# Kernel tuning notes

Hardware: AMD Instinct MI355X
Metric: run time of the kernel (lower is better)

## Reference

```python
import jax, jax.numpy as jnp
import numpy as np

NUM_HEAD = 16
DIM = 1024
T, B = 2048, 4


def setup_inputs() -> dict:
    key = jax.random.key(0)
    ks = jax.random.split(key, 12)
    s = 1.0 / np.sqrt(DIM)
    return {
        "x1": jax.random.normal(ks[0], (T, B, DIM), jnp.float32),
        "x2": jax.random.normal(ks[1], (T, B, DIM), jnp.float32),
        "Wq": jax.random.normal(ks[2], (DIM, DIM), jnp.float32) * s,
        "bq": jax.random.normal(ks[3], (DIM,), jnp.float32) * 0.01,
        "Wk": jax.random.normal(ks[4], (DIM, DIM), jnp.float32) * s,
        "bk": jax.random.normal(ks[5], (DIM,), jnp.float32) * 0.01,
        "Wv": jax.random.normal(ks[6], (DIM, DIM), jnp.float32) * s,
        "bv": jax.random.normal(ks[7], (DIM,), jnp.float32) * 0.01,
        "Wu": jax.random.normal(ks[8], (DIM, DIM), jnp.float32) * s,
        "bu": jax.random.normal(ks[9], (DIM,), jnp.float32) * 0.01,
    }


def reference(x1, x2, Wq, bq, Wk, bk, Wv, bv, Wu, bu):
    T1, B1, C = x1.shape
    T2 = x2.shape[0]
    H = NUM_HEAD
    hd = C // H
    # (T,B,C) -> (B,T,C)
    x1b = jnp.transpose(x1, (1, 0, 2))
    x2b = jnp.transpose(x2, (1, 0, 2))
    # torch Linear: y = x @ W.T + b
    q = (x1b @ Wq.T + bq).reshape(B1, T1, H, hd).transpose(0, 2, 1, 3)  # (B,H,T1,hd)
    k = (x2b @ Wk.T + bk).reshape(B1, T2, H, hd).transpose(0, 2, 1, 3)
    v = (x2b @ Wv.T + bv).reshape(B1, T2, H, hd).transpose(0, 2, 1, 3)
    # NOTE: source scales by 1/sqrt(C) (full dim), not 1/sqrt(head_dim)
    attn = jnp.einsum("bhqd,bhkd->bhqk", q, k) / jnp.sqrt(jnp.asarray(C, q.dtype))
    attn = jax.nn.softmax(attn, axis=-1)
    # dropout = identity (eval mode, deterministic reference)
    out = jnp.einsum("bhqk,bhkd->bhqd", attn, v)  # (B,H,T1,hd)
    out = out.transpose(0, 2, 1, 3).reshape(B1, T1, C)  # merge heads
    out = out @ Wu.T + bu
    return out
```

## Files before the change

### kernel.cpp

```cpp
#include <hip/hip_runtime.h>

#define TSEQ 2048
#define BB 4
#define CDIM 1024
#define NH 16
#define HD 64
#define MR (TSEQ*BB)
#define C2SCALE 0.045084220f

typedef __attribute__((ext_vector_type(8))) short sh8;
typedef __attribute__((ext_vector_type(4))) short sh4;
typedef __attribute__((ext_vector_type(4))) float f4;
typedef __attribute__((ext_vector_type(4))) unsigned int u32x4;

__device__ __forceinline__ unsigned short f2bf(float x){
  unsigned u = __builtin_bit_cast(unsigned, x);
  u += 0x7fffu + ((u>>16)&1u);
  return (unsigned short)(u>>16);
}

__device__ __forceinline__ unsigned cvtpk(float a, float b){
  unsigned r;
  asm("v_cvt_pk_bf16_f32 %0, %1, %2" : "=v"(r) : "v"(a), "v"(b));
  return r;
}

__device__ __forceinline__ void gll16(const unsigned short* g, unsigned short* l){
  __builtin_amdgcn_global_load_lds(
      (const __attribute__((address_space(1))) unsigned int*)g,
      (__attribute__((address_space(3))) unsigned int*)l, 16, 0, 0);
}

__global__ void conv_x(const float* __restrict__ a, const float* __restrict__ b,
                       unsigned short* __restrict__ ya, unsigned short* __restrict__ yb){
  const float* s = blockIdx.y ? b : a;
  unsigned short* d = blockIdx.y ? yb : ya;
  int i = (blockIdx.x*256 + threadIdx.x)*4;
  f4 v = *(const f4*)(s+i);
  sh4 o;
  o.x = (short)f2bf(v.x); o.y = (short)f2bf(v.y);
  o.z = (short)f2bf(v.z); o.w = (short)f2bf(v.w);
  *(sh4*)(d+i) = o;
}

__global__ void conv_w(const float* __restrict__ w0, const float* __restrict__ w1,
                       const float* __restrict__ w2, const float* __restrict__ w3,
                       unsigned short* __restrict__ y0, unsigned short* __restrict__ y1,
                       unsigned short* __restrict__ y2, unsigned short* __restrict__ y3){
  const float* s; unsigned short* d;
  switch(blockIdx.y){
    case 0: s=w0; d=y0; break;
    case 1: s=w1; d=y1; break;
    case 2: s=w2; d=y2; break;
    default: s=w3; d=y3; break;
  }
  int i = (blockIdx.x*256 + threadIdx.x)*4;
  f4 v = *(const f4*)(s+i);
  sh4 o;
  o.x = (short)f2bf(v.x); o.y = (short)f2bf(v.y);
  o.z = (short)f2bf(v.z); o.w = (short)f2bf(v.w);
  *(sh4*)(d+i) = o;
}

#define NKT 16
#define BUFS 24576

__device__ __forceinline__ void gemm_core(
    const unsigned short* __restrict__ Aglob, const unsigned short* __restrict__ Bglob,
    unsigned short* smem, int m0, int n0, int tid, f4 (&acc)[8][4])
{
  const int wave = tid>>6, lane = tid&63;
  const int g = lane>>4, c = lane&15;
  const int wr = wave>>1, wc = wave&1;

  const int srow = tid>>3, sch = tid&7;
  const unsigned short* aBase = Aglob + (size_t)(m0+srow)*CDIM + (sch^(srow&7))*8;
  const unsigned short* bBase = Bglob + (size_t)(n0+srow)*CDIM + (sch^(srow&7))*8;

#pragma unroll
  for (int i=0;i<8;i++) gll16(aBase + (size_t)i*32*CDIM,      smem + (i*256+tid)*8);
#pragma unroll
  for (int i=0;i<4;i++) gll16(bBase + (size_t)i*32*CDIM,      smem + 16384 + (i*256+tid)*8);
#pragma unroll
  for (int i=0;i<8;i++) gll16(aBase + (size_t)i*32*CDIM + 64, smem + BUFS + (i*256+tid)*8);
#pragma unroll
  for (int i=0;i<4;i++) gll16(bBase + (size_t)i*32*CDIM + 64, smem + BUFS + 16384 + (i*256+tid)*8);
  asm volatile("s_waitcnt vmcnt(12)" ::: "memory");
  __builtin_amdgcn_s_barrier();

  const int arow = wr*128 + c;
  const int brow = wc*64 + c;
  const int ch0 = g ^ (c&7);
  const int ch1 = (4+g) ^ (c&7);

  int q = 0;
  for (int kt=0; kt<NKT; kt++){
    unsigned short* bufc = smem + q*BUFS;
    int rr = q+2; if (rr>=3) rr-=3;
    unsigned short* dst = smem + rr*BUFS;
    if (kt+2 < NKT){
      const size_t koff = (size_t)(kt+2)*64;
#pragma unroll
      for (int i=0;i<8;i++) gll16(aBase + (size_t)i*32*CDIM + koff, dst + (i*256+tid)*8);
#pragma unroll
      for (int i=0;i<4;i++) gll16(bBase + (size_t)i*32*CDIM + koff, dst + 16384 + (i*256+tid)*8);
    }
    sh8 af[8][2], bfr[4][2];
#pragma unroll
    for (int mt=0;mt<8;mt++){
      af[mt][0] = *(const sh8*)(bufc + (arow+mt*16)*64 + ch0*8);
      af[mt][1] = *(const sh8*)(bufc + (arow+mt*16)*64 + ch1*8);
    }
#pragma unroll
    for (int nt=0;nt<4;nt++){
      bfr[nt][0] = *(const sh8*)(bufc + 16384 + (brow+nt*16)*64 + ch0*8);
      bfr[nt][1] = *(const sh8*)(bufc + 16384 + (brow+nt*16)*64 + ch1*8);
    }
    __builtin_amdgcn_s_setprio(1);
#pragma unroll
    for (int mt=0;mt<8;mt++)
#pragma unroll
      for (int nt=0;nt<4;nt++){
        acc[mt][nt] = __builtin_amdgcn_mfma_f32_16x16x32_bf16(af[mt][0], bfr[nt][0], acc[mt][nt],0,0,0);
        acc[mt][nt] = __builtin_amdgcn_mfma_f32_16x16x32_bf16(af[mt][1], bfr[nt][1], acc[mt][nt],0,0,0);
      }
    __builtin_amdgcn_s_setprio(0);
    if (kt < NKT-1){
      if (kt < NKT-2) asm volatile("s_waitcnt vmcnt(12)" ::: "memory");
      else            asm volatile("s_waitcnt vmcnt(0)" ::: "memory");
    }
    __builtin_amdgcn_s_barrier();
    q = (q==2)?0:q+1;
  }
}

__global__ __launch_bounds__(256,1) void gemm_u(
    const unsigned short* __restrict__ A, const unsigned short* __restrict__ Bw,
    const float* __restrict__ bias, float* __restrict__ Cout){
  __shared__ unsigned short smem[3*BUFS];
  const int tid  = threadIdx.x;
  const int wave = tid>>6, lane = tid&63;
  const int g = lane>>4, c = lane&15;
  const int m0 = blockIdx.x*256, n0 = blockIdx.y*128;
  const int wr = wave>>1, wc = wave&1;
  f4 acc[8][4] = {};
  gemm_core(A, Bw, smem, m0, n0, tid, acc);

#pragma unroll
  for (int nt=0; nt<4; nt++){
    int nn = n0 + wc*64 + nt*16 + c;
    float bsv = bias[nn];
#pragma unroll
    for (int mt=0; mt<8; mt++){
      int mb = m0 + wr*128 + mt*16 + 4*g;
#pragma unroll
      for (int r=0; r<4; r++)
        Cout[(size_t)(mb+r)*CDIM + nn] = acc[mt][nt][r] + bsv;
    }
  }
}

__global__ __launch_bounds__(256,1) void gemm_qkv(
    const unsigned short* __restrict__ x1b, const unsigned short* __restrict__ x2b,
    const unsigned short* __restrict__ wq, const unsigned short* __restrict__ wk,
    const unsigned short* __restrict__ wv,
    const float* __restrict__ bq, const float* __restrict__ bk, const float* __restrict__ bv,
    unsigned short* __restrict__ Qo, unsigned short* __restrict__ Ko,
    unsigned short* __restrict__ Vo){
  __shared__ unsigned short smem[3*BUFS];
  const int z = blockIdx.z;
  const unsigned short* A  = (z==0) ? x1b : x2b;
  const unsigned short* Bw = (z==0) ? wq : (z==1) ? wk : wv;
  const float* bias        = (z==0) ? bq : (z==1) ? bk : bv;
  const int tid  = threadIdx.x;
  const int wave = tid>>6, lane = tid&63;
  const int g = lane>>4, c = lane&15;
  const int m0 = blockIdx.x*256, n0 = blockIdx.y*128;
  const int wr = wave>>1, wc = wave&1;
  f4 acc[8][4] = {};
  gemm_core(A, Bw, smem, m0, n0, tid, acc);

#pragma unroll
  for (int nt=0; nt<4; nt++){
    int nn = n0 + wc*64 + nt*16 + c;
    float bsv = bias[nn];
#pragma unroll
    for (int mt=0; mt<8; mt++){
      int mb = m0 + wr*128 + mt*16 + 4*g;
#pragma unroll
      for (int r=0; r<4; r++){
        float v = acc[mt][nt][r] + bsv;
        int mm = mb + r;
        if (z==0){
          Qo[(size_t)mm*CDIM + nn] = f2bf(v*C2SCALE);
        } else if (z==1){
          Ko[(size_t)mm*CDIM + nn] = f2bf(v);
        } else {
          int t = mm>>2, bb = mm&3, h = nn>>6, d = nn&63;
          Vo[(((size_t)bb*NH + h)*HD + d)*TSEQ + t] = f2bf(v);
        }
      }
    }
  }
}

__global__ __launch_bounds__(256,4) void attn_kernel(
    const unsigned short* __restrict__ Q, const unsigned short* __restrict__ Kb,
    const unsigned short* __restrict__ Vt, unsigned short* __restrict__ O){
  __shared__ unsigned short Ks[2][64*64];
  __shared__ unsigned short Vs[2][64*64];
  const int tid=threadIdx.x, wave=tid>>6, lane=tid&63;
  const int g=lane>>4, c=lane&15;
  const bool godd = (g&1);
  const int gx = blockIdx.x;
  const int bh = ((gx>>7)<<3) | (gx&7);
  const int qt = (gx>>3)&15;
  const int b = bh>>4, h = bh&15;
  const int qbase = qt*128 + wave*32;

  u32x4 onesw; onesw.x=0x3f803f80u; onesw.y=0x3f803f80u; onesw.z=0x3f803f80u; onesw.w=0x3f803f80u;
  const sh8 vones = __builtin_bit_cast(sh8, onesw);

  const unsigned short* kb0[2];
  const unsigned short* vb0[2];
#pragma unroll
  for (int i=0; i<2; i++){
    int cc = i*256+tid;
    int krow = cc>>3, kch = (cc&7) ^ (krow&7);
    kb0[i] = Kb + ((size_t)krow*BB + b)*CDIM + h*HD + kch*8;
    int vd = cc>>3, vch = (cc&7) ^ (vd&7);
    vb0[i] = Vt + ((size_t)(b*NH+h)*HD + vd)*TSEQ + vch*8;
  }

  sh8 qfr[2][2];
#pragma unroll
  for (int qf=0; qf<2; qf++)
#pragma unroll
    for (int kc=0; kc<2; kc++){
      int t = qbase + qf*16 + c;
      qfr[qf][kc] = *(const sh8*)(Q + ((size_t)t*BB + b)*CDIM + h*HD + kc*32 + g*8);
    }

  f4 oacc[4][2] = {};
  f4 dacc[2] = {};

#pragma unroll
  for (int i=0; i<2; i++){
    gll16(kb0[i], Ks[0] + (i*256+tid)*8);
    gll16(vb0[i], Vs[0] + (i*256+tid)*8);
  }
  __syncthreads();

  const int NT = TSEQ/64;
  int cur = 0;
  for (int it=0; it<NT; it++){
    if (it+1 < NT){
      int k0n = (it+1)*64;
#pragma unroll
      for (int i=0; i<2; i++){
        gll16(kb0[i] + (size_t)k0n*BB*CDIM, Ks[cur^1] + (i*256+tid)*8);
        gll16(vb0[i] + k0n,                 Vs[cur^1] + (i*256+tid)*8);
      }
    }
    const unsigned short* ks = Ks[cur];
    const unsigned short* vs = Vs[cur];

#pragma unroll
    for (int sub=0; sub<2; sub++){
      f4 sacc[2][2] = {};
      __builtin_amdgcn_s_setprio(1);
#pragma unroll
      for (int j=0; j<2; j++){
        int kf = sub*2 + j;
        sh8 af[2];
#pragma unroll
        for (int kc=0; kc<2; kc++){
          int ch = (kc*4+g) ^ (c&7);
          af[kc] = *(const sh8*)(ks + (kf*16+c)*64 + ch*8);
        }
#pragma unroll
        for (int kc=0; kc<2; kc++)
#pragma unroll
          for (int qf=0; qf<2; qf++)
            sacc[j][qf] = __builtin_amdgcn_mfma_f32_16x16x32_bf16(af[kc], qfr[qf][kc], sacc[j][qf],0,0,0);
      }
      __builtin_amdgcn_s_setprio(0);

      sh8 pf[2];
#pragma unroll
      for (int qf=0; qf<2; qf++){
        f4 sa = sacc[0][qf];
        f4 sb = sacc[1][qf];
        float pa0 = __builtin_amdgcn_exp2f(sa[0]);
        float pa1 = __builtin_amdgcn_exp2f(sa[1]);
        float pa2 = __builtin_amdgcn_exp2f(sa[2]);
        float pa3 = __builtin_amdgcn_exp2f(sa[3]);
        float pb0 = __builtin_amdgcn_exp2f(sb[0]);
        float pb1 = __builtin_amdgcn_exp2f(sb[1]);
        float pb2 = __builtin_amdgcn_exp2f(sb[2]);
        float pb3 = __builtin_amdgcn_exp2f(sb[3]);
        unsigned A0 = cvtpk(pa0, pa1);
        unsigned A1 = cvtpk(pa2, pa3);
        unsigned B0 = cvtpk(pb0, pb1);
        unsigned B1 = cvtpk(pb2, pb3);
        asm("v_permlane32_swap_b32 %0, %1" : "+v"(A0), "+v"(B0));
        asm("v_permlane32_swap_b32 %0, %1" : "+v"(A1), "+v"(B1));
        unsigned xA0 = (unsigned)__builtin_amdgcn_ds_swizzle((int)A0, 0x401F);
        unsigned xA1 = (unsigned)__builtin_amdgcn_ds_swizzle((int)A1, 0x401F);
        unsigned xB0 = (unsigned)__builtin_amdgcn_ds_swizzle((int)B0, 0x401F);
        unsigned xB1 = (unsigned)__builtin_amdgcn_ds_swizzle((int)B1, 0x401F);
        u32x4 pw;
        pw.x = godd ? xB0 : A0;
        pw.y = godd ? xB1 : A1;
        pw.z = godd ? B0  : xA0;
        pw.w = godd ? B1  : xA1;
        pf[qf] = __builtin_bit_cast(sh8, pw);
      }
      __builtin_amdgcn_s_setprio(1);
#pragma unroll
      for (int qf=0; qf<2; qf++)
        dacc[qf] = __builtin_amdgcn_mfma_f32_16x16x32_bf16(vones, pf[qf], dacc[qf],0,0,0);
#pragma unroll
      for (int df=0; df<4; df++){
        int ch = (sub*4+g) ^ (c&7);
        sh8 vf = *(const sh8*)(vs + (df*16+c)*64 + ch*8);
#pragma unroll
        for (int qf=0; qf<2; qf++)
          oacc[df][qf] = __builtin_amdgcn_mfma_f32_16x16x32_bf16(vf, pf[qf], oacc[df][qf],0,0,0);
      }
      __builtin_amdgcn_s_setprio(0);
    }

    __syncthreads();
    cur ^= 1;
  }

#pragma unroll
  for (int qf=0; qf<2; qf++){
    float inv = 1.0f/dacc[qf][0];
    int t = qbase + qf*16 + c;
#pragma unroll
    for (int df=0; df<4; df++){
      uint2 pr;
      pr.x = cvtpk(oacc[df][qf][0]*inv, oacc[df][qf][1]*inv);
      pr.y = cvtpk(oacc[df][qf][2]*inv, oacc[df][qf][3]*inv);
      *(uint2*)(O + ((size_t)b*TSEQ + t)*CDIM + h*HD + df*16 + 4*g) = pr;
    }
  }
}

extern "C" void kernel_launch(void* const* d_in, const int* in_sizes, int n_in,
                              void* d_out, int out_size, void* d_ws, size_t ws_size,
                              hipStream_t stream){
  (void)in_sizes; (void)n_in; (void)out_size; (void)ws_size;
  const float* x1 = (const float*)d_in[0];
  const float* x2 = (const float*)d_in[1];
  const float* Wq = (const float*)d_in[2];
  const float* bq = (const float*)d_in[3];
  const float* Wk = (const float*)d_in[4];
  const float* bk = (const float*)d_in[5];
  const float* Wv = (const float*)d_in[6];
  const float* bv = (const float*)d_in[7];
  const float* Wu = (const float*)d_in[8];
  const float* bu = (const float*)d_in[9];

  unsigned short* ws = (unsigned short*)d_ws;
  size_t o = 0;
  unsigned short* x1b = ws + o; o += (size_t)MR*CDIM;
  unsigned short* x2b = ws + o; o += (size_t)MR*CDIM;
  unsigned short* wqb = ws + o; o += (size_t)CDIM*CDIM;
  unsigned short* wkb = ws + o; o += (size_t)CDIM*CDIM;
  unsigned short* wvb = ws + o; o += (size_t)CDIM*CDIM;
  unsigned short* wub = ws + o; o += (size_t)CDIM*CDIM;
  unsigned short* Qb  = ws + o; o += (size_t)MR*CDIM;
  unsigned short* Kbf = ws + o; o += (size_t)MR*CDIM;
  unsigned short* Vtb = ws + o; o += (size_t)MR*CDIM;
  unsigned short* Ob  = x1b;

  conv_x<<<dim3((MR*CDIM)/1024, 2),   256, 0, stream>>>(x1, x2, x1b, x2b);
  conv_w<<<dim3((CDIM*CDIM)/1024, 4), 256, 0, stream>>>(Wq, Wk, Wv, Wu, wqb, wkb, wvb, wub);

  gemm_qkv<<<dim3(MR/256, CDIM/128, 3), 256, 0, stream>>>(
      x1b, x2b, wqb, wkb, wvb, bq, bk, bv, Qb, Kbf, Vtb);
  attn_kernel<<<dim3(1024), 256, 0, stream>>>(Qb, Kbf, Vtb, Ob);
  gemm_u<<<dim3(MR/256, CDIM/128), 256, 0, stream>>>(Ob, wub, bu, (float*)d_out);
}
```

Baseline: 325.4 us.

## Halve GEMM k-slab to fit two blocks per CU; compute softmax denominator with VALU sums

The shared GEMM core now stages 32-wide k slabs (half the LDS per stage) with a 4-chunk swizzle and 32 pipeline steps. The QKV and output GEMMs move to launch_bounds(256,2) so two blocks can share a CU. Separately, the attention kernel drops the ones-vector MFMA used for the row sum. It accumulates the fp32 exponentials in registers and reduces them across lane groups with shuffles at the end. The trade-offs are more loop iterations and barriers in the GEMM, and a possible register squeeze from the occupancy bound against the 8x4 accumulator tile.

New measurement: 318.5 us. -2.1%, faster.

```diff
diff --git a/kernel.cpp b/kernel.cpp
--- a/kernel.cpp
+++ b/kernel.cpp
@@ -62,8 +62,8 @@
   *(sh4*)(d+i) = o;
 }
 
-#define NKT 16
-#define BUFS 24576
+#define NST 32
+#define SLOT 12288
 
 __device__ __forceinline__ void gemm_core(
     const unsigned short* __restrict__ Aglob, const unsigned short* __restrict__ Bglob,
@@ -73,71 +73,70 @@
   const int g = lane>>4, c = lane&15;
   const int wr = wave>>1, wc = wave&1;
 
-  const int srow = tid>>3, sch = tid&7;
-  const unsigned short* aBase = Aglob + (size_t)(m0+srow)*CDIM + (sch^(srow&7))*8;
-  const unsigned short* bBase = Bglob + (size_t)(n0+srow)*CDIM + (sch^(srow&7))*8;
-
-#pragma unroll
-  for (int i=0;i<8;i++) gll16(aBase + (size_t)i*32*CDIM,      smem + (i*256+tid)*8);
-#pragma unroll
-  for (int i=0;i<4;i++) gll16(bBase + (size_t)i*32*CDIM,      smem + 16384 + (i*256+tid)*8);
-#pragma unroll
-  for (int i=0;i<8;i++) gll16(aBase + (size_t)i*32*CDIM + 64, smem + BUFS + (i*256+tid)*8);
-#pragma unroll
-  for (int i=0;i<4;i++) gll16(bBase + (size_t)i*32*CDIM + 64, smem + BUFS + 16384 + (i*256+tid)*8);
-  asm volatile("s_waitcnt vmcnt(12)" ::: "memory");
+  const unsigned short* aSrc[4]; int aOff[4];
+  const unsigned short* bSrc[2]; int bOff[2];
+#pragma unroll
+  for (int i=0;i<4;i++){
+    int slot = i*256+tid; int row = slot>>2, ch = slot&3;
+    aSrc[i] = Aglob + (size_t)(m0+row)*CDIM + (ch ^ ((row>>1)&3))*8;
+    aOff[i] = slot*8;
+  }
+#pragma unroll
+  for (int i=0;i<2;i++){
+    int slot = i*256+tid; int row = slot>>2, ch = slot&3;
+    bSrc[i] = Bglob + (size_t)(n0+row)*CDIM + (ch ^ ((row>>1)&3))*8;
+    bOff[i] = 8192 + slot*8;
+  }
+  const int swz = (c>>1)&3;
+  const int aro = (wr*128 + c)*32 + (g ^ swz)*8;
+  const int bro = 8192 + (wc*64 + c)*32 + (g ^ swz)*8;
+
+#pragma unroll
+  for (int i=0;i<4;i++) gll16(aSrc[i],    smem + aOff[i]);
+#pragma unroll
+  for (int i=0;i<2;i++) gll16(bSrc[i],    smem + bOff[i]);
+#pragma unroll
+  for (int i=0;i<4;i++) gll16(aSrc[i]+32, smem + SLOT + aOff[i]);
+#pragma unroll
+  for (int i=0;i<2;i++) gll16(bSrc[i]+32, smem + SLOT + bOff[i]);
+  asm volatile("s_waitcnt vmcnt(6)" ::: "memory");
   __builtin_amdgcn_s_barrier();
 
-  const int arow = wr*128 + c;
-  const int brow = wc*64 + c;
-  const int ch0 = g ^ (c&7);
-  const int ch1 = (4+g) ^ (c&7);
-
   int q = 0;
-  for (int kt=0; kt<NKT; kt++){
-    unsigned short* bufc = smem + q*BUFS;
+  for (int s=0; s<NST; s++){
+    unsigned short* bufc = smem + q*SLOT;
     int rr = q+2; if (rr>=3) rr-=3;
-    unsigned short* dst = smem + rr*BUFS;
-    if (kt+2 < NKT){
-      const size_t koff = (size_t)(kt+2)*64;
-#pragma unroll
-      for (int i=0;i<8;i++) gll16(aBase + (size_t)i*32*CDIM + koff, dst + (i*256+tid)*8);
-#pragma unroll
-      for (int i=0;i<4;i++) gll16(bBase + (size_t)i*32*CDIM + koff, dst + 16384 + (i*256+tid)*8);
-    }
-    sh8 af[8][2], bfr[4][2];
-#pragma unroll
-    for (int mt=0;mt<8;mt++){
-      af[mt][0] = *(const sh8*)(bufc + (arow+mt*16)*64 + ch0*8);
-      af[mt][1] = *(const sh8*)(bufc + (arow+mt*16)*64 + ch1*8);
-    }
-#pragma unroll
-    for (int nt=0;nt<4;nt++){
-      bfr[nt][0] = *(const sh8*)(bufc + 16384 + (brow+nt*16)*64 + ch0*8);
-      bfr[nt][1] = *(const sh8*)(bufc + 16384 + (brow+nt*16)*64 + ch1*8);
-    }
+    unsigned short* dst = smem + rr*SLOT;
+    if (s+2 < NST){
+      const int ko = (s+2)*32;
+#pragma unroll
+      for (int i=0;i<4;i++) gll16(aSrc[i]+ko, dst + aOff[i]);
+#pragma unroll
+      for (int i=0;i<2;i++) gll16(bSrc[i]+ko, dst + bOff[i]);
+    }
+    sh8 af[8], bfr[4];
+#pragma unroll
+    for (int mt=0;mt<8;mt++) af[mt]  = *(const sh8*)(bufc + aro + mt*512);
+#pragma unroll
+    for (int nt=0;nt<4;nt++) bfr[nt] = *(const sh8*)(bufc + bro + nt*512);
     __builtin_amdgcn_s_setprio(1);
 #pragma unroll
     for (int mt=0;mt<8;mt++)
 #pragma unroll
-      for (int nt=0;nt<4;nt++){
-        acc[mt][nt] = __builtin_amdgcn_mfma_f32_16x16x32_bf16(af[mt][0], bfr[nt][0], acc[mt][nt],0,0,0);
-        acc[mt][nt] = __builtin_amdgcn_mfma_f32_16x16x32_bf16(af[mt][1], bfr[nt][1], acc[mt][nt],0,0,0);
-      }
+      for (int nt=0;nt<4;nt++)
+        acc[mt][nt] = __builtin_amdgcn_mfma_f32_16x16x32_bf16(af[mt], bfr[nt], acc[mt][nt],0,0,0);
     __builtin_amdgcn_s_setprio(0);
-    if (kt < NKT-1){
-      if (kt < NKT-2) asm volatile("s_waitcnt vmcnt(12)" ::: "memory");
-      else            asm volatile("s_waitcnt vmcnt(0)" ::: "memory");
-    }
+    if (s < NST-2)       asm volatile("s_waitcnt vmcnt(6)" ::: "memory");
+    else if (s == NST-2) asm volatile("s_waitcnt vmcnt(0)" ::: "memory");
     __builtin_amdgcn_s_barrier();
     q = (q==2)?0:q+1;
   }
 }
 
-__global__ __launch_bounds__(256,1) void gemm_u(
+__global__ __launch_bounds__(256,2) void gemm_u(
     const unsigned short* __restrict__ A, const unsigned short* __restrict__ Bw,
     const float* __restrict__ bias, float* __restrict__ Cout){
-  __shared__ unsigned short smem[3*BUFS];
+  __shared__ unsigned short smem[3*SLOT];
   const int tid  = threadIdx.x;
   const int wave = tid>>6, lane = tid&63;
   const int g = lane>>4, c = lane&15;
@@ -160,14 +159,14 @@
   }
 }
 
-__global__ __launch_bounds__(256,1) void gemm_qkv(
+__global__ __launch_bounds__(256,2) void gemm_qkv(
     const unsigned short* __restrict__ x1b, const unsigned short* __restrict__ x2b,
     const unsigned short* __restrict__ wq, const unsigned short* __restrict__ wk,
     const unsigned short* __restrict__ wv,
     const float* __restrict__ bq, const float* __restrict__ bk, const float* __restrict__ bv,
     unsigned short* __restrict__ Qo, unsigned short* __restrict__ Ko,
     unsigned short* __restrict__ Vo){
-  __shared__ unsigned short smem[3*BUFS];
+  __shared__ unsigned short smem[3*SLOT];
   const int z = blockIdx.z;
   const unsigned short* A  = (z==0) ? x1b : x2b;
   const unsigned short* Bw = (z==0) ? wq : (z==1) ? wk : wv;
@@ -218,9 +217,6 @@
   const int b = bh>>4, h = bh&15;
   const int qbase = qt*128 + wave*32;
 
-  u32x4 onesw; onesw.x=0x3f803f80u; onesw.y=0x3f803f80u; onesw.z=0x3f803f80u; onesw.w=0x3f803f80u;
-  const sh8 vones = __builtin_bit_cast(sh8, onesw);
-
   const unsigned short* kb0[2];
   const unsigned short* vb0[2];
 #pragma unroll
@@ -242,7 +238,7 @@
     }
 
   f4 oacc[4][2] = {};
-  f4 dacc[2] = {};
+  float lrun[2] = {0.f, 0.f};
 
 #pragma unroll
   for (int i=0; i<2; i++){
@@ -299,6 +295,7 @@
         float pb1 = __builtin_amdgcn_exp2f(sb[1]);
         float pb2 = __builtin_amdgcn_exp2f(sb[2]);
         float pb3 = __builtin_amdgcn_exp2f(sb[3]);
+        lrun[qf] += ((pa0+pa1)+(pa2+pa3)) + ((pb0+pb1)+(pb2+pb3));
         unsigned A0 = cvtpk(pa0, pa1);
         unsigned A1 = cvtpk(pa2, pa3);
         unsigned B0 = cvtpk(pb0, pb1);
@@ -318,9 +315,6 @@
       }
       __builtin_amdgcn_s_setprio(1);
 #pragma unroll
-      for (int qf=0; qf<2; qf++)
-        dacc[qf] = __builtin_amdgcn_mfma_f32_16x16x32_bf16(vones, pf[qf], dacc[qf],0,0,0);
-#pragma unroll
       for (int df=0; df<4; df++){
         int ch = (sub*4+g) ^ (c&7);
         sh8 vf = *(const sh8*)(vs + (df*16+c)*64 + ch*8);
@@ -337,7 +331,9 @@
 
 #pragma unroll
   for (int qf=0; qf<2; qf++){
-    float inv = 1.0f/dacc[qf][0];
+    lrun[qf] += __shfl_xor(lrun[qf], 16, 64);
+    lrun[qf] += __shfl_xor(lrun[qf], 32, 64);
+    float inv = 1.0f/lrun[qf];
     int t = qbase + qf*16 + c;
 #pragma unroll
     for (int df=0; df<4; df++){
```
